# Optimization experiments

Measured on AMD Instinct MI355X. Metric: run time of the kernel, lower is better.

Reference implementation:

```python
import jax, jax.numpy as jnp
import numpy as np

P, K, C = 16, 256, 3          # patches, boxes per patch, classes
PATCH = 1024                   # patch size (px)
SIZE_FACTOR = 1.0
IOU_T = 0.55                   # wbf_iou_thresh
PRE = P * K                    # pre_wbf_detections = 4096
POST = 1000                    # max_detections


def setup_inputs() -> dict:
    key = jax.random.key(0)
    k1, k2, k3, k4, k5, k6 = jax.random.split(key, 6)
    # realistic xyxy boxes inside a 1024px patch, 8..56 px wide
    cx = jax.random.uniform(k1, (P, K)) * (PATCH - 64)
    cy = jax.random.uniform(k2, (P, K)) * (PATCH - 64)
    w = jax.random.uniform(k3, (P, K)) * 48.0 + 8.0
    h = jax.random.uniform(k4, (P, K)) * 48.0 + 8.0
    b4 = jnp.stack([cx, cy, cx + w, cy + h], axis=-1)          # [P,K,4]
    scores = jax.random.uniform(k5, (P, K, 1))                  # (0,1)
    labels = jax.random.randint(k6, (P, K, 1), 0, C).astype(jnp.float32)
    boxes = jnp.concatenate([b4, scores, labels], axis=-1)      # [P,K,6]
    stride = float(int(PATCH * 0.8))
    grid = jnp.arange(4, dtype=jnp.float32) * stride
    ox = jnp.tile(grid, 4)
    oy = jnp.repeat(grid, 4)
    offsets = jnp.stack([ox, oy], axis=-1)                      # [P,2] (xmin,ymin)
    return {"boxes": boxes, "offsets": offsets}


def _wbf(dets):
    """Greedy class-aware weighted boxes fusion.

    dets: [N,6] = (x1,y1,x2,y2,score,label). Sequential scan: each box joins
    the first existing cluster of the SAME class with IoU(merged_box)>IOU_T,
    else opens a new cluster. Class-aware matching inside one scan is
    math-equivalent to the original per-class loops (clusters never mix
    classes; within-class order is preserved; output is score-sorted anyway).
    """
    N = dets.shape[0]
    init = (
        jnp.zeros((N, 4), jnp.float32),   # mbox: current merged box per slot
        jnp.zeros((N, 4), jnp.float32),   # wsum: sum(score*box)
        jnp.zeros((N,), jnp.float32),     # ssum: sum(score)
        jnp.zeros((N,), jnp.float32),     # cnt:  members per cluster
        jnp.full((N,), -1.0, jnp.float32),# cls:  cluster class id
        jnp.array(0, jnp.int32),          # num:  clusters opened so far
    )

    def step(carry, row):
        mbox, wsum, ssum, cnt, cls, num = carry
        box, score, label = row[:4], row[4], row[5]
        # IoU of `box` against every cluster slot (vectorized)
        xx1 = jnp.maximum(mbox[:, 0], box[0])
        yy1 = jnp.maximum(mbox[:, 1], box[1])
        xx2 = jnp.minimum(mbox[:, 2], box[2])
        yy2 = jnp.minimum(mbox[:, 3], box[3])
        inter = jnp.clip(xx2 - xx1, 0.0) * jnp.clip(yy2 - yy1, 0.0)
        area_a = (box[2] - box[0]) * (box[3] - box[1])
        area_b = (mbox[:, 2] - mbox[:, 0]) * (mbox[:, 3] - mbox[:, 1])
        union = area_a + area_b - inter
        iou = jnp.where(union > 0.0, inter / union, 0.0)
        match = (cnt > 0) & (cls == label) & (iou > IOU_T)
        has = jnp.any(match)
        idx = jnp.where(has, jnp.argmax(match).astype(jnp.int32), num)
        wsum = wsum.at[idx].add(score * box)
        ssum = ssum.at[idx].add(score)
        cnt = cnt.at[idx].add(1.0)
        mbox = mbox.at[idx].set(wsum[idx] / ssum[idx])
        cls = cls.at[idx].set(label)
        num = num + jnp.where(has, 0, 1).astype(jnp.int32)
        return (mbox, wsum, ssum, cnt, cls, num), None

    (mbox, wsum, ssum, cnt, cls, num), _ = jax.lax.scan(step, init, dets)
    valid = cnt > 0.0
    scores = jnp.where(valid, ssum / jnp.maximum(cnt, 1.0), 0.0)  # mean score
    return mbox, scores, cls, valid


def reference(boxes, offsets):
    # PatchMerger: shift boxes into global coords, rescale by size_factor
    off4 = jnp.concatenate([offsets, offsets], axis=-1)[:, None, :]  # [P,1,4]
    b4 = (boxes[..., :4] + off4) / SIZE_FACTOR                       # [P,K,4]
    dets = jnp.concatenate([b4, boxes[..., 4:]], axis=-1).reshape(-1, 6)[:PRE]
    # WBF clustering
    mbox, scores, cls, valid = _wbf(dets)
    # sort by score desc, keep top POST; pad rows zeroed
    sort_key = jnp.where(valid, scores, -1.0)
    topv, topi = jax.lax.top_k(sort_key, POST)
    out = jnp.concatenate([mbox, scores[:, None], cls[:, None]], axis=-1)[topi]
    out = jnp.where((topv >= 0.0)[:, None], out, 0.0)
    return out  # [POST, 6]
```

## Files before the change

kernel.cpp:

```cpp
#include <hip/hip_runtime.h>

#define N 4096
#define NT 1024
#define BATCH 64
#define KCAND 8
#define IOU_THR 0.55f
#define INF 0x7fffffff
#define NBINS 14
#define NBKT 42
#define BCAP 320

__device__ float4 g_wsum[N];

__device__ __forceinline__ float rl_f(float v, int lane) {
  return __int_as_float(__builtin_amdgcn_readlane(__float_as_int(v), lane));
}
__device__ __forceinline__ int rl_i(int v, int lane) {
  return __builtin_amdgcn_readlane(v, lane);
}

__global__ __launch_bounds__(NT) void wbf_kernel(
    const float* __restrict__ boxes,
    const float* __restrict__ offs,
    float* __restrict__ out)
{
  __shared__ float4 s_mbox[N];
  __shared__ float  s_ssum[N];
  __shared__ unsigned short s_cc[N];
  __shared__ unsigned s_gate32[N];
  __shared__ unsigned short s_bkt[NBKT][BCAP];
  __shared__ int s_bktlen[NBKT];
  __shared__ uint4 s_cand4[BATCH];
  __shared__ int   s_ccnt[BATCH];
  __shared__ __align__(16) float s_batch[BATCH][8];
  __shared__ unsigned s_bgate[BATCH];
  __shared__ unsigned long long s_pm[BATCH];
  __shared__ int s_min[2];
  __shared__ int s_num, s_resume, s_ovf;

  const int tid = threadIdx.x;

  if (tid < NBKT) s_bktlen[tid] = 0;
  if (tid == 0) { s_num = 0; s_resume = BATCH; s_ovf = 0; s_min[0] = INF; s_min[1] = INF; }

  for (int t0 = 0; t0 < N; t0 += BATCH) {
    if (tid < BATCH) {
      int gi = t0 + tid;
      const float* br = boxes + (size_t)gi * 6;
      int p = gi >> 8;
      float ox = offs[2 * p], oy = offs[2 * p + 1];
      float x1 = br[0] + ox, y1 = br[1] + oy;
      float x2 = br[2] + ox, y2 = br[3] + oy;
      float sc = br[4], lb = br[5];
      s_batch[tid][0] = x1; s_batch[tid][1] = y1;
      s_batch[tid][2] = x2; s_batch[tid][3] = y2;
      s_batch[tid][4] = sc; s_batch[tid][5] = lb;
      s_bgate[tid] = ((unsigned)(((int)lb << 12) | (int)x1) << 16) | (unsigned)(int)y1;
    } else if (tid < 2 * BATCH) {
      s_ccnt[tid - BATCH] = 0;
    } else if (tid < 3 * BATCH) {
      s_pm[tid - 2 * BATCH] = 0ull;
    }
    __syncthreads();

    int nm0 = s_num;
    int use_linear = s_ovf;

    if (!use_linear) {
      int b = tid >> 4, sl = tid & 15;
      float qx1 = s_batch[b][0], qy1 = s_batch[b][1];
      float qx2 = s_batch[b][2], qy2 = s_batch[b][3];
      int cls = (int)s_batch[b][5];
      unsigned qxq = (unsigned)(int)qx1, qyq = (unsigned)(int)qy1;
      float aA = (qx2 - qx1) * (qy2 - qy1);
      int bb = ((int)qx1) >> 8;
      int jlo = bb > 0 ? bb - 1 : 0;
      int jhi = bb < NBINS - 1 ? bb + 1 : NBINS - 1;
      for (int j = jlo; j <= jhi; ++j) {
        int bk = cls * NBINS + j;
        int len = s_bktlen[bk]; if (len > BCAP) len = BCAP;
        for (int e = sl; e < len; e += 16) {
          int c = (int)s_bkt[bk][e];
          unsigned g = s_gate32[c];
          unsigned dx = __usad(g >> 16, qxq, 0u);
          unsigned dy = __usad(g & 0xFFFFu, qyq, 0u);
          if (dx <= 60u && dy <= 60u) {
            float4 m = s_mbox[c];
            float xx1 = fmaxf(m.x, qx1), yy1 = fmaxf(m.y, qy1);
            float xx2 = fminf(m.z, qx2), yy2 = fminf(m.w, qy2);
            float iw = fmaxf(xx2 - xx1, 0.0f), ih = fmaxf(yy2 - yy1, 0.0f);
            float inter = iw * ih;
            float aB = (m.z - m.x) * (m.w - m.y);
            float uni = aA + aB - inter;
            if (uni > 0.0f && inter / uni > IOU_THR) {
              int pos = atomicAdd(&s_ccnt[b], 1);
              if (pos < KCAND) ((unsigned short*)&s_cand4[b])[pos] = (unsigned short)c;
            }
          }
        }
      }
    } else {
      for (int c = tid; c < nm0; c += NT) {
        float4 m = s_mbox[c];
        int mcls = (int)(s_cc[c] >> 14);
        float aB = (m.z - m.x) * (m.w - m.y);
        for (int b2 = 0; b2 < BATCH; ++b2) {
          float qx1 = s_batch[b2][0], qy1 = s_batch[b2][1];
          if (fabsf(m.x - qx1) < 60.0f && fabsf(m.y - qy1) < 60.0f &&
              mcls == (int)s_batch[b2][5]) {
            float qx2 = s_batch[b2][2], qy2 = s_batch[b2][3];
            float xx1 = fmaxf(m.x, qx1), yy1 = fmaxf(m.y, qy1);
            float xx2 = fminf(m.z, qx2), yy2 = fminf(m.w, qy2);
            float iw = fmaxf(xx2 - xx1, 0.0f), ih = fmaxf(yy2 - yy1, 0.0f);
            float inter = iw * ih;
            float aA = (qx2 - qx1) * (qy2 - qy1);
            float uni = aA + aB - inter;
            if (uni > 0.0f && inter / uni > IOU_THR) {
              int pos = atomicAdd(&s_ccnt[b2], 1);
              if (pos < KCAND) ((unsigned short*)&s_cand4[b2])[pos] = (unsigned short)c;
            }
          }
        }
      }
    }
    #pragma unroll
    for (int q = 0; q < 4; ++q) {
      int p = tid + q * NT;
      int bb2 = p >> 6, jj = p & 63;
      if (jj < bb2) {
        unsigned gb = s_bgate[bb2], gj = s_bgate[jj];
        unsigned dx = __usad(gb >> 16, gj >> 16, 0u);
        unsigned dy = __usad(gb & 0xFFFFu, gj & 0xFFFFu, 0u);
        if (dx <= 60u && dy <= 60u) {
          float ax1 = s_batch[bb2][0], ay1 = s_batch[bb2][1];
          float ax2 = s_batch[bb2][2], ay2 = s_batch[bb2][3];
          float jx1 = s_batch[jj][0], jy1 = s_batch[jj][1];
          float jx2 = s_batch[jj][2], jy2 = s_batch[jj][3];
          float xx1 = fmaxf(ax1, jx1), yy1 = fmaxf(ay1, jy1);
          float xx2 = fminf(ax2, jx2), yy2 = fminf(ay2, jy2);
          float iw = fmaxf(xx2 - xx1, 0.0f), ih = fmaxf(yy2 - yy1, 0.0f);
          float inter = iw * ih;
          float aA = (ax2 - ax1) * (ay2 - ay1);
          float aB = (jx2 - jx1) * (jy2 - jy1);
          float uni = aA + aB - inter;
          if (uni > 0.0f && inter / uni > IOU_THR)
            atomicOr(&s_pm[bb2], 1ull << jj);
        }
      }
    }
    __syncthreads();

    if (tid < 64) {
      const int lane = tid;
      float4 qa = *(const float4*)&s_batch[lane][0];
      float2 qb = *(const float2*)&s_batch[lane][4];
      float p0 = qa.x, p1 = qa.y, p2 = qa.z, p3 = qa.w, p4 = qb.x, p5 = qb.y;
      int   cc_l = s_ccnt[lane];
      uint4 cp_l = s_cand4[lane];
      unsigned long long pm_l = s_pm[lane];
      int pml_lo = (int)(unsigned)pm_l, pml_hi = (int)(unsigned)(pm_l >> 32);
      int c0 = (int)(cp_l.x & 0xFFFFu);
      float4 wp0 = make_float4(0.f, 0.f, 0.f, 0.f);
      float ssp0 = 1.0f; int ctp0 = 0;
      if (cc_l > 0) { wp0 = g_wsum[c0]; ssp0 = s_ssum[c0]; ctp0 = (int)s_cc[c0]; }

      unsigned dlo = 0u, dhi = 0u;

      unsigned long long anycand = __ballot(cc_l > 0);
      unsigned long long OVF = __ballot(cc_l > KCAND);
      unsigned long long F = __ballot(cc_l > 0 || pm_l != 0ull);
      int rs = BATCH;
      if (OVF) rs = (int)__builtin_ctzll(OVF);
      unsigned long long lowrs = (rs >= 64) ? ~0ull : ((1ull << rs) - 1ull);
      unsigned long long rem = F & lowrs;
      unsigned long long NEWM = ~F & lowrs;
      unsigned long long consumed = 0ull;

      int nmod = 0;
      int e_valid = 0, e_idx = INF, e_ct = 0, e_origbb = -1;
      float e_cls = -1.0f;
      float e_m0=0,e_m1=0,e_m2=0,e_m3=0, e_w0=0,e_w1=0,e_w2=0,e_w3=0, e_ss=0;

      while (rem) {
        int b = (int)__builtin_ctzll(rem);
        rem &= rem - 1ull;
        float bx1 = rl_f(p0, b), by1 = rl_f(p1, b);
        float bx2 = rl_f(p2, b), by2 = rl_f(p3, b);
        float sc  = rl_f(p4, b), lbf = rl_f(p5, b);

        int v = INF;
        if (e_valid && e_cls == lbf &&
            fabsf(e_m0 - bx1) < 60.0f && fabsf(e_m1 - by1) < 60.0f) {
          float xx1 = fmaxf(e_m0, bx1), yy1 = fmaxf(e_m1, by1);
          float xx2 = fminf(e_m2, bx2), yy2 = fminf(e_m3, by2);
          float iw = fmaxf(xx2 - xx1, 0.0f), ih = fmaxf(yy2 - yy1, 0.0f);
          float inter = iw * ih;
          float aA = (bx2 - bx1) * (by2 - by1);
          float aB = (e_m2 - e_m0) * (e_m3 - e_m1);
          float uni = aA + aB - inter;
          if (uni > 0.0f && inter / uni > IOU_THR) v = e_idx;
        }
        if ((anycand >> b) & 1ull) {
          int cc = rl_i(cc_l, b);
          unsigned w0 = (unsigned)rl_i((int)cp_l.x, b);
          unsigned w1 = (unsigned)rl_i((int)cp_l.y, b);
          unsigned w2 = (unsigned)rl_i((int)cp_l.z, b);
          unsigned w3 = (unsigned)rl_i((int)cp_l.w, b);
          unsigned w = (lane >= 6) ? w3 : (lane >= 4) ? w2 : (lane >= 2) ? w1 : w0;
          int ci = (int)((w >> ((lane & 1) * 16)) & 0xFFFFu);
          int widx = (ci >> 6) & 63;
          unsigned dl = (unsigned)__builtin_amdgcn_ds_bpermute(widx << 2, (int)dlo);
          unsigned dh = (unsigned)__builtin_amdgcn_ds_bpermute(widx << 2, (int)dhi);
          unsigned word = (ci & 32) ? dh : dl;
          if (lane < cc && !((word >> (ci & 31)) & 1u)) v = min(v, ci);
        }
        unsigned long long ball = __ballot(v != INF);
        int mn = INF;
        if (ball != 0ull) {
          if (__popcll(ball) == 1) {
            mn = rl_i(v, (int)__builtin_ctzll(ball));
          } else {
            int t = v;
            for (int o = 32; o; o >>= 1) t = min(t, __shfl_xor(t, o));
            mn = t;
          }
        }
        unsigned long long pc =
            (((unsigned long long)(unsigned)rl_i(pml_hi, b)) << 32) |
            (unsigned long long)(unsigned)rl_i(pml_lo, b);
        pc &= ~F & ~consumed;
        int pj = 64, pairidx = INF;
        if (pc) {
          pj = (int)__builtin_ctzll(pc);
          pairidx = nm0 + (int)__builtin_popcountll(NEWM & ((1ull << pj) - 1ull));
        }
        if (pairidx < mn) mn = pairidx;

        if (mn == INF) {
          int nidx = nm0 + (int)__builtin_popcountll(NEWM & ((1ull << b) - 1ull));
          NEWM |= 1ull << b;
          if (lane == nmod) {
            e_valid = 1; e_idx = nidx; e_cls = lbf; e_origbb = -1;
            e_w0 = sc * bx1; e_w1 = sc * by1; e_w2 = sc * bx2; e_w3 = sc * by2;
            e_ss = sc; e_ct = 1;
            e_m0 = e_w0 / e_ss; e_m1 = e_w1 / e_ss; e_m2 = e_w2 / e_ss; e_m3 = e_w3 / e_ss;
          }
          nmod++;
        } else {
          bool mine = e_valid && (e_idx == mn);
          unsigned long long mb = __ballot(mine);
          int owner;
          if (mb != 0ull) {
            owner = (int)__builtin_ctzll(mb);
            if (mine) {
              e_w0 += sc * bx1; e_w1 += sc * by1; e_w2 += sc * bx2; e_w3 += sc * by2;
              e_ss += sc; e_ct += 1;
              e_m0 = e_w0 / e_ss; e_m1 = e_w1 / e_ss; e_m2 = e_w2 / e_ss; e_m3 = e_w3 / e_ss;
            }
          } else if (mn < nm0) {
            owner = nmod;
            int rc0 = rl_i(c0, b);
            if (lane == nmod) {
              float w0, w1, w2, w3, ss; int ctp;
              if (mn == rc0) {
                w0 = rl_f(wp0.x, b); w1 = rl_f(wp0.y, b);
                w2 = rl_f(wp0.z, b); w3 = rl_f(wp0.w, b);
                ss = rl_f(ssp0, b);  ctp = rl_i(ctp0, b);
              } else {
                float4 w = g_wsum[mn];
                w0 = w.x; w1 = w.y; w2 = w.z; w3 = w.w;
                ss = s_ssum[mn]; ctp = (int)s_cc[mn];
              }
              e_valid = 1; e_idx = mn; e_cls = lbf;
              e_origbb = ((int)(w0 / ss)) >> 8;
              e_w0 = w0 + sc * bx1; e_w1 = w1 + sc * by1;
              e_w2 = w2 + sc * bx2; e_w3 = w3 + sc * by2;
              e_ss = ss + sc; e_ct = (ctp & 0x3FFF) + 1;
              e_m0 = e_w0 / e_ss; e_m1 = e_w1 / e_ss; e_m2 = e_w2 / e_ss; e_m3 = e_w3 / e_ss;
            }
            if (lane == ((mn >> 6) & 63)) {
              if (mn & 32) dhi |= 1u << (mn & 31); else dlo |= 1u << (mn & 31);
            }
            nmod++;
          } else {
            owner = nmod;
            consumed |= 1ull << pj;
            if (lane == nmod) {
              float jx1 = rl_f(p0, pj), jy1 = rl_f(p1, pj);
              float jx2 = rl_f(p2, pj), jy2 = rl_f(p3, pj);
              float jsc = rl_f(p4, pj);
              e_valid = 1; e_idx = mn; e_cls = lbf; e_origbb = -1;
              e_w0 = jsc * jx1 + sc * bx1; e_w1 = jsc * jy1 + sc * by1;
              e_w2 = jsc * jx2 + sc * bx2; e_w3 = jsc * jy2 + sc * by2;
              e_ss = jsc + sc; e_ct = 2;
              e_m0 = e_w0 / e_ss; e_m1 = e_w1 / e_ss; e_m2 = e_w2 / e_ss; e_m3 = e_w3 / e_ss;
            }
            nmod++;
          }
          float nx1 = rl_f(e_m0, owner), ny1 = rl_f(e_m1, owner);
          float nx2 = rl_f(e_m2, owner), ny2 = rl_f(e_m3, owner);
          bool dp = false;
          if (p5 == lbf) {
            float xx1 = fmaxf(nx1, p0), yy1 = fmaxf(ny1, p1);
            float xx2 = fminf(nx2, p2), yy2 = fminf(ny2, p3);
            float iw = fmaxf(xx2 - xx1, 0.0f), ih = fmaxf(yy2 - yy1, 0.0f);
            float inter = iw * ih;
            float aA = (p2 - p0) * (p3 - p1);
            float aB = (nx2 - nx1) * (ny2 - ny1);
            float uni = aA + aB - inter;
            dp = (uni > 0.0f) && (inter / uni > IOU_THR);
          }
          unsigned long long det = __ballot(dp);
          unsigned long long himask = (b >= 63) ? 0ull : (~0ull << (b + 1));
          det &= ~F & ~consumed & lowrs & himask;
          if (det) { F |= det; rem |= det; NEWM &= ~det; }
        }
      }

      if (e_valid) {
        s_mbox[e_idx] = make_float4(e_m0, e_m1, e_m2, e_m3);
        g_wsum[e_idx] = make_float4(e_w0, e_w1, e_w2, e_w3);
        s_ssum[e_idx] = e_ss;
        s_cc[e_idx] = (unsigned short)(e_ct | (((int)e_cls) << 14));
        s_gate32[e_idx] = ((unsigned)(int)e_m0 << 16) | (unsigned)(int)e_m1;
        int nb = ((int)e_m0) >> 8;
        if (nb < 0) nb = 0; if (nb > NBINS - 1) nb = NBINS - 1;
        if (nb != e_origbb) {
          int bk = ((int)e_cls) * NBINS + nb;
          int p = atomicAdd(&s_bktlen[bk], 1);
          if (p < BCAP) s_bkt[bk][p] = (unsigned short)e_idx; else s_ovf = 1;
        }
      }
      {
        unsigned long long selfbit = 1ull << lane;
        if (NEWM & ~F & ~consumed & selfbit) {
          int idx = nm0 + (int)__builtin_popcountll(NEWM & (selfbit - 1ull));
          float w0 = p4 * p0, w1 = p4 * p1, w2 = p4 * p2, w3 = p4 * p3;
          float m0 = w0 / p4, m1 = w1 / p4, m2 = w2 / p4, m3 = w3 / p4;
          g_wsum[idx] = make_float4(w0, w1, w2, w3);
          s_ssum[idx] = p4;
          s_cc[idx] = (unsigned short)(1 | (((int)p5) << 14));
          s_mbox[idx] = make_float4(m0, m1, m2, m3);
          s_gate32[idx] = ((unsigned)(int)m0 << 16) | (unsigned)(int)m1;
          int nb = ((int)m0) >> 8;
          if (nb < 0) nb = 0; if (nb > NBINS - 1) nb = NBINS - 1;
          int bk = ((int)p5) * NBINS + nb;
          int p = atomicAdd(&s_bktlen[bk], 1);
          if (p < BCAP) s_bkt[bk][p] = (unsigned short)idx; else s_ovf = 1;
        }
      }
      if (lane == 0) {
        s_num = nm0 + (int)__builtin_popcountll(NEWM);
        s_resume = rs;
      }
    }
    __syncthreads();

    int rs2 = s_resume;
    if (rs2 < BATCH) {
      for (int i = rs2; i < BATCH; ++i) {
        float bx1 = s_batch[i][0], by1 = s_batch[i][1];
        float bx2 = s_batch[i][2], by2 = s_batch[i][3];
        float sc  = s_batch[i][4];
        int lb = (int)s_batch[i][5];
        int nm = s_num;
        float aA = (bx2 - bx1) * (by2 - by1);
        int mymin = INF;
        for (int c = tid; c < nm; c += NT) {
          float4 m = s_mbox[c];
          if (fabsf(m.x - bx1) < 60.0f && fabsf(m.y - by1) < 60.0f &&
              (int)(s_cc[c] >> 14) == lb) {
            float xx1 = fmaxf(m.x, bx1), yy1 = fmaxf(m.y, by1);
            float xx2 = fminf(m.z, bx2), yy2 = fminf(m.w, by2);
            float iw = fmaxf(xx2 - xx1, 0.0f), ih = fmaxf(yy2 - yy1, 0.0f);
            float inter = iw * ih;
            float aB = (m.z - m.x) * (m.w - m.y);
            float uni = aA + aB - inter;
            if (uni > 0.0f && inter / uni > IOU_THR) mymin = min(mymin, c);
          }
        }
        if (mymin != INF) atomicMin(&s_min[i & 1], mymin);
        __syncthreads();
        int mn = s_min[i & 1];
        if (tid == 0) {
          s_min[(i + 1) & 1] = INF;
          bool has = (mn != INF);
          int idx = has ? mn : nm;
          float w0, w1, w2, w3, ss; int ct, ob = -1;
          if (has) {
            float4 w = g_wsum[idx];
            w0 = w.x; w1 = w.y; w2 = w.z; w3 = w.w;
            ss = s_ssum[idx]; ct = (int)(s_cc[idx] & 0x3FFF);
            ob = ((int)s_mbox[idx].x) >> 8;
          } else { w0 = w1 = w2 = w3 = 0.0f; ss = 0.0f; ct = 0; }
          w0 += sc * bx1; w1 += sc * by1; w2 += sc * bx2; w3 += sc * by2;
          ss += sc; ct += 1;
          float m0 = w0 / ss, m1 = w1 / ss, m2 = w2 / ss, m3 = w3 / ss;
          g_wsum[idx] = make_float4(w0, w1, w2, w3);
          s_ssum[idx] = ss;
          s_cc[idx] = (unsigned short)(ct | (lb << 14));
          s_mbox[idx] = make_float4(m0, m1, m2, m3);
          s_gate32[idx] = ((unsigned)(int)m0 << 16) | (unsigned)(int)m1;
          int nb = ((int)m0) >> 8;
          if (nb < 0) nb = 0; if (nb > NBINS - 1) nb = NBINS - 1;
          if (nb != ob) {
            int bk = lb * NBINS + nb;
            int p = atomicAdd(&s_bktlen[bk], 1);
            if (p < BCAP) s_bkt[bk][p] = (unsigned short)idx; else s_ovf = 1;
          }
          if (!has) s_num = nm + 1;
        }
        __syncthreads();
      }
      if (tid == 0) { s_min[0] = INF; s_min[1] = INF; }
    }
  }

  __syncthreads();
  unsigned long long* s_keys = (unsigned long long*)s_mbox;
  int num = s_num;
  for (int j = tid; j < N; j += NT) {
    unsigned int lo = ~(unsigned int)j;
    unsigned long long key;
    if (j < num) {
      float ct = (float)(s_cc[j] & 0x3FFF);
      float sco = s_ssum[j] / fmaxf(ct, 1.0f);
      unsigned int bb = __float_as_uint(sco) | 0x80000000u;
      key = ((unsigned long long)bb << 32) | lo;
    } else {
      key = (0x407FFFFFull << 32) | lo;
    }
    s_keys[j] = key;
  }
  __syncthreads();

  for (int k = 2; k <= N; k <<= 1) {
    for (int j = k >> 1; j > 0; j >>= 1) {
      #pragma unroll
      for (int w = 0; w < N / NT; ++w) {
        int a0 = tid + (w << 10);
        int l = a0 ^ j;
        if (l > a0) {
          unsigned long long a = s_keys[a0], bq = s_keys[l];
          bool desc = ((a0 & k) == 0);
          bool sw = desc ? (a < bq) : (a > bq);
          if (sw) { s_keys[a0] = bq; s_keys[l] = a; }
        }
      }
      __syncthreads();
    }
  }

  if (tid < 1000) {
    unsigned long long key = s_keys[tid];
    unsigned int hi = (unsigned int)(key >> 32);
    float* o = out + (size_t)tid * 6;
    if (hi & 0x80000000u) {
      int j = (int)(~(unsigned int)key);
      float4 w = g_wsum[j];
      float ss = s_ssum[j];
      o[0] = w.x / ss; o[1] = w.y / ss; o[2] = w.z / ss; o[3] = w.w / ss;
      o[4] = __uint_as_float(hi & 0x7FFFFFFFu);
      o[5] = (float)(s_cc[j] >> 14);
    } else {
      o[0] = 0.0f; o[1] = 0.0f; o[2] = 0.0f;
      o[3] = 0.0f; o[4] = 0.0f; o[5] = 0.0f;
    }
  }
}

extern "C" void kernel_launch(void* const* d_in, const int* in_sizes, int n_in,
                              void* d_out, int out_size, void* d_ws, size_t ws_size,
                              hipStream_t stream) {
  const float* boxes = (const float*)d_in[0];
  const float* offs  = (const float*)d_in[1];
  float* out = (float*)d_out;
  hipLaunchKernelGGL(wbf_kernel, dim3(1), dim3(NT), 0, stream, boxes, offs, out);
}
```

Measured before the change: 325.9 us.

## Use fast reciprocals, LDS dirty bitmap, and min-candidate prefetch in WBF wave loop

Replaces the IEEE divisions in merged-box updates with a hardware reciprocal multiply. Moves the dirty-cluster tracking from register bitmaps read with ds_bpermute to a shared-memory bitmap that is only checked once any cluster is dirty. Prefetches the smallest candidate's sums instead of the first one, and narrows the s_batch row from 8 to 6 floats. Together these aim to shorten the serial single-wave scan. The approximate reciprocal can shift IoU results and merged coordinates slightly, and the unaligned rows replace vector loads with scalar ones.

```diff
diff --git a/kernel.cpp b/kernel.cpp
--- a/kernel.cpp
+++ b/kernel.cpp
@@ -18,6 +18,7 @@
 __device__ __forceinline__ int rl_i(int v, int lane) {
   return __builtin_amdgcn_readlane(v, lane);
 }
+__device__ __forceinline__ float frcp(float x) { return __builtin_amdgcn_rcpf(x); }
 
 __global__ __launch_bounds__(NT) void wbf_kernel(
     const float* __restrict__ boxes,
@@ -30,9 +31,10 @@
   __shared__ unsigned s_gate32[N];
   __shared__ unsigned short s_bkt[NBKT][BCAP];
   __shared__ int s_bktlen[NBKT];
+  __shared__ unsigned long long s_dirty[64];
   __shared__ uint4 s_cand4[BATCH];
   __shared__ int   s_ccnt[BATCH];
-  __shared__ __align__(16) float s_batch[BATCH][8];
+  __shared__ float s_batch[BATCH][6];
   __shared__ unsigned s_bgate[BATCH];
   __shared__ unsigned long long s_pm[BATCH];
   __shared__ int s_min[2];
@@ -40,6 +42,7 @@
 
   const int tid = threadIdx.x;
 
+  if (tid < 64) s_dirty[tid] = 0ull;
   if (tid < NBKT) s_bktlen[tid] = 0;
   if (tid == 0) { s_num = 0; s_resume = BATCH; s_ovf = 0; s_min[0] = INF; s_min[1] = INF; }
 
@@ -152,29 +155,34 @@
 
     if (tid < 64) {
       const int lane = tid;
-      float4 qa = *(const float4*)&s_batch[lane][0];
-      float2 qb = *(const float2*)&s_batch[lane][4];
-      float p0 = qa.x, p1 = qa.y, p2 = qa.z, p3 = qa.w, p4 = qb.x, p5 = qb.y;
+      float p0 = s_batch[lane][0], p1 = s_batch[lane][1], p2 = s_batch[lane][2];
+      float p3 = s_batch[lane][3], p4 = s_batch[lane][4], p5 = s_batch[lane][5];
       int   cc_l = s_ccnt[lane];
       uint4 cp_l = s_cand4[lane];
       unsigned long long pm_l = s_pm[lane];
       int pml_lo = (int)(unsigned)pm_l, pml_hi = (int)(unsigned)(pm_l >> 32);
-      int c0 = (int)(cp_l.x & 0xFFFFu);
+
+      const unsigned short* cl = (const unsigned short*)&cp_l;
+      int lim = cc_l < KCAND ? cc_l : KCAND;
+      int mnl = INF;
+      #pragma unroll
+      for (int k = 0; k < KCAND; ++k)
+        if (k < lim) mnl = min(mnl, (int)cl[k]);
       float4 wp0 = make_float4(0.f, 0.f, 0.f, 0.f);
       float ssp0 = 1.0f; int ctp0 = 0;
-      if (cc_l > 0) { wp0 = g_wsum[c0]; ssp0 = s_ssum[c0]; ctp0 = (int)s_cc[c0]; }
-
-      unsigned dlo = 0u, dhi = 0u;
+      if (cc_l > 0) { wp0 = g_wsum[mnl]; ssp0 = s_ssum[mnl]; ctp0 = (int)s_cc[mnl]; }
 
       unsigned long long anycand = __ballot(cc_l > 0);
       unsigned long long OVF = __ballot(cc_l > KCAND);
-      unsigned long long F = __ballot(cc_l > 0 || pm_l != 0ull);
+      unsigned long long PAIRS = __ballot(pm_l != 0ull);
+      unsigned long long F = anycand | PAIRS;
       int rs = BATCH;
       if (OVF) rs = (int)__builtin_ctzll(OVF);
       unsigned long long lowrs = (rs >= 64) ? ~0ull : ((1ull << rs) - 1ull);
       unsigned long long rem = F & lowrs;
       unsigned long long NEWM = ~F & lowrs;
       unsigned long long consumed = 0ull;
+      bool anydirty = false;
 
       int nmod = 0;
       int e_valid = 0, e_idx = INF, e_ct = 0, e_origbb = -1;
@@ -206,13 +214,13 @@
           unsigned w1 = (unsigned)rl_i((int)cp_l.y, b);
           unsigned w2 = (unsigned)rl_i((int)cp_l.z, b);
           unsigned w3 = (unsigned)rl_i((int)cp_l.w, b);
-          unsigned w = (lane >= 6) ? w3 : (lane >= 4) ? w2 : (lane >= 2) ? w1 : w0;
-          int ci = (int)((w >> ((lane & 1) * 16)) & 0xFFFFu);
-          int widx = (ci >> 6) & 63;
-          unsigned dl = (unsigned)__builtin_amdgcn_ds_bpermute(widx << 2, (int)dlo);
-          unsigned dh = (unsigned)__builtin_amdgcn_ds_bpermute(widx << 2, (int)dhi);
-          unsigned word = (ci & 32) ? dh : dl;
-          if (lane < cc && !((word >> (ci & 31)) & 1u)) v = min(v, ci);
+          if (lane < cc) {
+            unsigned w = (lane >= 6) ? w3 : (lane >= 4) ? w2 : (lane >= 2) ? w1 : w0;
+            int ci = (int)((w >> ((lane & 1) * 16)) & 0xFFFFu);
+            bool clean = true;
+            if (anydirty) clean = !((s_dirty[ci >> 6] >> (ci & 63)) & 1ull);
+            if (clean) v = min(v, ci);
+          }
         }
         unsigned long long ball = __ballot(v != INF);
         int mn = INF;
@@ -243,7 +251,8 @@
             e_valid = 1; e_idx = nidx; e_cls = lbf; e_origbb = -1;
             e_w0 = sc * bx1; e_w1 = sc * by1; e_w2 = sc * bx2; e_w3 = sc * by2;
             e_ss = sc; e_ct = 1;
-            e_m0 = e_w0 / e_ss; e_m1 = e_w1 / e_ss; e_m2 = e_w2 / e_ss; e_m3 = e_w3 / e_ss;
+            float r = frcp(e_ss);
+            e_m0 = e_w0 * r; e_m1 = e_w1 * r; e_m2 = e_w2 * r; e_m3 = e_w3 * r;
           }
           nmod++;
         } else {
@@ -255,14 +264,16 @@
             if (mine) {
               e_w0 += sc * bx1; e_w1 += sc * by1; e_w2 += sc * bx2; e_w3 += sc * by2;
               e_ss += sc; e_ct += 1;
-              e_m0 = e_w0 / e_ss; e_m1 = e_w1 / e_ss; e_m2 = e_w2 / e_ss; e_m3 = e_w3 / e_ss;
+              float r = frcp(e_ss);
+              e_m0 = e_w0 * r; e_m1 = e_w1 * r; e_m2 = e_w2 * r; e_m3 = e_w3 * r;
             }
           } else if (mn < nm0) {
             owner = nmod;
-            int rc0 = rl_i(c0, b);
+            anydirty = true;
+            int rmn = rl_i(mnl, b);
             if (lane == nmod) {
               float w0, w1, w2, w3, ss; int ctp;
-              if (mn == rc0) {
+              if (mn == rmn) {
                 w0 = rl_f(wp0.x, b); w1 = rl_f(wp0.y, b);
                 w2 = rl_f(wp0.z, b); w3 = rl_f(wp0.w, b);
                 ss = rl_f(ssp0, b);  ctp = rl_i(ctp0, b);
@@ -272,14 +283,13 @@
                 ss = s_ssum[mn]; ctp = (int)s_cc[mn];
               }
               e_valid = 1; e_idx = mn; e_cls = lbf;
-              e_origbb = ((int)(w0 / ss)) >> 8;
+              e_origbb = ((int)(w0 * frcp(ss))) >> 8;
               e_w0 = w0 + sc * bx1; e_w1 = w1 + sc * by1;
               e_w2 = w2 + sc * bx2; e_w3 = w3 + sc * by2;
               e_ss = ss + sc; e_ct = (ctp & 0x3FFF) + 1;
-              e_m0 = e_w0 / e_ss; e_m1 = e_w1 / e_ss; e_m2 = e_w2 / e_ss; e_m3 = e_w3 / e_ss;
-            }
-            if (lane == ((mn >> 6) & 63)) {
-              if (mn & 32) dhi |= 1u << (mn & 31); else dlo |= 1u << (mn & 31);
+              float r = frcp(e_ss);
+              e_m0 = e_w0 * r; e_m1 = e_w1 * r; e_m2 = e_w2 * r; e_m3 = e_w3 * r;
+              atomicOr(&s_dirty[mn >> 6], 1ull << (mn & 63));
             }
             nmod++;
           } else {
@@ -293,7 +303,8 @@
               e_w0 = jsc * jx1 + sc * bx1; e_w1 = jsc * jy1 + sc * by1;
               e_w2 = jsc * jx2 + sc * bx2; e_w3 = jsc * jy2 + sc * by2;
               e_ss = jsc + sc; e_ct = 2;
-              e_m0 = e_w0 / e_ss; e_m1 = e_w1 / e_ss; e_m2 = e_w2 / e_ss; e_m3 = e_w3 / e_ss;
+              float r = frcp(e_ss);
+              e_m0 = e_w0 * r; e_m1 = e_w1 * r; e_m2 = e_w2 * r; e_m3 = e_w3 * r;
             }
             nmod++;
           }
@@ -336,7 +347,8 @@
         if (NEWM & ~F & ~consumed & selfbit) {
           int idx = nm0 + (int)__builtin_popcountll(NEWM & (selfbit - 1ull));
           float w0 = p4 * p0, w1 = p4 * p1, w2 = p4 * p2, w3 = p4 * p3;
-          float m0 = w0 / p4, m1 = w1 / p4, m2 = w2 / p4, m3 = w3 / p4;
+          float r = frcp(p4);
+          float m0 = w0 * r, m1 = w1 * r, m2 = w2 * r, m3 = w3 * r;
           g_wsum[idx] = make_float4(w0, w1, w2, w3);
           s_ssum[idx] = p4;
           s_cc[idx] = (unsigned short)(1 | (((int)p5) << 14));
@@ -349,6 +361,7 @@
           if (p < BCAP) s_bkt[bk][p] = (unsigned short)idx; else s_ovf = 1;
         }
       }
+      s_dirty[lane] = 0ull;
       if (lane == 0) {
         s_num = nm0 + (int)__builtin_popcountll(NEWM);
         s_resume = rs;
@@ -395,7 +408,8 @@
           } else { w0 = w1 = w2 = w3 = 0.0f; ss = 0.0f; ct = 0; }
           w0 += sc * bx1; w1 += sc * by1; w2 += sc * bx2; w3 += sc * by2;
           ss += sc; ct += 1;
-          float m0 = w0 / ss, m1 = w1 / ss, m2 = w2 / ss, m3 = w3 / ss;
+          float r = frcp(ss);
+          float m0 = w0 * r, m1 = w1 * r, m2 = w2 * r, m3 = w3 * r;
           g_wsum[idx] = make_float4(w0, w1, w2, w3);
           s_ssum[idx] = ss;
           s_cc[idx] = (unsigned short)(ct | (lb << 14));
```

Result: no change. 325.5 us (-0.1%).
